# Optimization experiments

Measured on AMD Instinct MI355X. Metric: run time of the kernel, lower is better.

The kernel has to match this reference:

```python
import jax, jax.numpy as jnp
import numpy as np

B, T, D, U, OUT = 64, 1024, 512, 512, 4

def setup_inputs() -> dict:
    key = jax.random.key(0)
    ks = jax.random.split(key, 6)
    s = lambda n: 1.0 / np.sqrt(n)
    return {
        "tx": jax.random.normal(ks[0], (B, T, D), dtype=jnp.float32),
        "kernel": jax.random.normal(ks[1], (D, 4 * U), dtype=jnp.float32) * s(D),
        "recurrent_kernel": jax.random.normal(ks[2], (U, 4 * U), dtype=jnp.float32) * s(U),
        "bias": jnp.zeros((4 * U,), dtype=jnp.float32),
        "fc_w": jax.random.normal(ks[3], (U, OUT), dtype=jnp.float32) * s(U),
        "fc_b": jnp.zeros((OUT,), dtype=jnp.float32),
    }

def reference(tx, kernel, recurrent_kernel, bias, fc_w, fc_b):
    b, t, d = tx.shape
    u = recurrent_kernel.shape[0]
    # Fuse the 4 per-gate input matmuls into one GEMM over all timesteps: [B,T,4U]
    xz = jnp.einsum('btd,dk->btk', tx, kernel) + bias

    def step(carry, xz_t):
        h, c = carry
        z = xz_t + h @ recurrent_kernel  # fused 4 recurrent matmuls
        z1, z2, z3, z4 = jnp.split(z, 4, axis=-1)
        v1 = jnp.tanh(z1)
        v2 = jax.nn.sigmoid(z2)
        v3 = jax.nn.sigmoid(z3)
        v4 = jax.nn.sigmoid(z4)
        c = v1 * v2 + v3 * c
        h = v4 * jnp.tanh(c)
        return (h, c), None

    h0 = jnp.zeros((b, u), dtype=tx.dtype)
    c0 = jnp.zeros((b, u), dtype=tx.dtype)
    (h_last, _), _ = jax.lax.scan(step, (h0, c0), jnp.swapaxes(xz, 0, 1))
    # RNN(return_sequences=False) -> last hidden state, then Dense + softmax
    return jax.nn.softmax(h_last @ fc_w + fc_b, axis=-1)
```

## Files before the change

### kernel.cpp

```cpp
#include <hip/hip_runtime.h>
#include <stdint.h>

typedef short sv8 __attribute__((ext_vector_type(8)));
typedef float fv4 __attribute__((ext_vector_type(4)));
typedef uint32_t u32x4 __attribute__((ext_vector_type(4)));
typedef uint32_t u32x2 __attribute__((ext_vector_type(2)));

__device__ __forceinline__ uint16_t f2bf(float f) {
    uint32_t u = __builtin_bit_cast(uint32_t, f);
    u += 0x7FFFu + ((u >> 16) & 1u);
    return (uint16_t)(u >> 16);
}
__device__ __forceinline__ float bf2f(uint16_t h) {
    uint32_t u = ((uint32_t)h) << 16;
    return __builtin_bit_cast(float, u);
}
__device__ __forceinline__ void split4(float4 f, ushort4& h, ushort4& l) {
    h.x = f2bf(f.x); l.x = f2bf(f.x - bf2f(h.x));
    h.y = f2bf(f.y); l.y = f2bf(f.y - bf2f(h.y));
    h.z = f2bf(f.z); l.z = f2bf(f.z - bf2f(h.z));
    h.w = f2bf(f.w); l.w = f2bf(f.w - bf2f(h.w));
}
__device__ __forceinline__ float fsig(float x)  { return 1.f / (1.f + __expf(-x)); }
__device__ __forceinline__ float ftanh(float x) { return 1.f - 2.f / (__expf(2.f * x) + 1.f); }

__device__ __forceinline__ u32x4 load16_cc(const void* p) {
    u32x4 r;
    asm volatile("global_load_dwordx4 %0, %1, off sc0 sc1" : "=v"(r) : "v"(p) : "memory");
    return r;
}
__device__ __forceinline__ uint32_t load4_cc(const void* p) {
    uint32_t r;
    asm volatile("global_load_dword %0, %1, off sc0 sc1" : "=v"(r) : "v"(p) : "memory");
    return r;
}
__device__ __forceinline__ void atom8_st(void* p, u32x2 v) {
    asm volatile("global_atomic_swap_x2 %0, %1, off" :: "v"(p), "v"(v) : "memory");
}
__device__ __forceinline__ void atom4_st(void* p, uint32_t v) {
    asm volatile("global_atomic_swap %0, %1, off" :: "v"(p), "v"(v) : "memory");
}

#define TT     1024
#define DD     512
#define NN     2048
#define TCH    128
#define NCHUNK 8
#define NREG   8
#define RSTRIDE 16

__global__ void prep_split_b(const float* __restrict__ kern,
                             uint16_t* __restrict__ bth, uint16_t* __restrict__ btl) {
    int tid = blockIdx.x * 256 + threadIdx.x;
    if (tid >= DD * NN) return;
    int k = tid >> 11;
    int n = tid & (NN - 1);
    float v = kern[tid];
    uint16_t h = f2bf(v);
    bth[n * DD + k] = h;
    btl[n * DD + k] = f2bf(v - bf2f(h));
}

__global__ void prep_rk(const float* __restrict__ rk,
                        uint16_t* __restrict__ rkh, uint16_t* __restrict__ rkl) {
    int tid = blockIdx.x * 256 + threadIdx.x;
    if (tid >= 128 * 16 * 64 * 8) return;
    int j = tid & 7, lane = (tid >> 3) & 63, kt = (tid >> 9) & 15, g = tid >> 13;
    int lq = lane >> 4, c = lane & 15;
    int k = kt * 32 + lq * 8 + j;
    int colg = (c >> 2) * 512 + g * 4 + (c & 3);
    float v = rk[(size_t)k * NN + colg];
    uint16_t h = f2bf(v);
    rkh[tid] = h;
    rkl[tid] = f2bf(v - bf2f(h));
}

__device__ __forceinline__ void gemm_tile(
    const float* __restrict__ tx, int t0,
    const uint16_t* __restrict__ Bth, const uint16_t* __restrict__ Btl,
    float* __restrict__ xz, uint16_t* sb, int t256, int btile, int n0, int act) {
    int lane = t256 & 63, w = t256 >> 6;
    int wm = (w >> 1) * 64, wn = (w & 1) * 64;
    int srow = t256 >> 1, scol = (t256 & 1) * 16;
    fv4 acc[4][4];
#pragma unroll
    for (int q = 0; q < 4; q++)
#pragma unroll
        for (int r = 0; r < 4; r++) acc[q][r] = (fv4){0.f, 0.f, 0.f, 0.f};

    const float* abase = tx + ((size_t)btile * TT + t0 + srow) * DD + scol;

    for (int k0 = 0; k0 < DD; k0 += 32) {
        float4 f0, f1, f2, f3;
        uint4 b0, b1, c0, c1;
        if (act) {
            const float4* A4 = (const float4*)(abase + k0);
            f0 = A4[0]; f1 = A4[1]; f2 = A4[2]; f3 = A4[3];
            const uint16_t* pb  = Bth + (size_t)(n0 + srow) * DD + k0 + scol;
            const uint16_t* pbl = Btl + (size_t)(n0 + srow) * DD + k0 + scol;
            b0 = *(const uint4*)pb;  b1 = *(const uint4*)(pb + 8);
            c0 = *(const uint4*)pbl; c1 = *(const uint4*)(pbl + 8);
        }
        __syncthreads();
        if (act) {
            union { ushort4 v4[4]; uint4 q[2]; } H, L;
            split4(f0, H.v4[0], L.v4[0]);
            split4(f1, H.v4[1], L.v4[1]);
            split4(f2, H.v4[2], L.v4[2]);
            split4(f3, H.v4[3], L.v4[3]);
            *(uint4*)&sb[srow * 32 + scol]            = H.q[0];
            *(uint4*)&sb[srow * 32 + scol + 8]        = H.q[1];
            *(uint4*)&sb[4096 + srow * 32 + scol]     = L.q[0];
            *(uint4*)&sb[4096 + srow * 32 + scol + 8] = L.q[1];
            *(uint4*)&sb[8192 + srow * 32 + scol]     = b0;
            *(uint4*)&sb[8192 + srow * 32 + scol + 8] = b1;
            *(uint4*)&sb[12288 + srow * 32 + scol]    = c0;
            *(uint4*)&sb[12288 + srow * 32 + scol + 8]= c1;
        }
        __syncthreads();
        sv8 ah[4], al[4], bh[4], bl[4];
#pragma unroll
        for (int q = 0; q < 4; q++) {
            int ra = (wm + q * 16 + (lane & 15)) * 32 + (lane >> 4) * 8;
            ah[q] = *(const sv8*)&sb[ra];
            al[q] = *(const sv8*)&sb[4096 + ra];
        }
#pragma unroll
        for (int r = 0; r < 4; r++) {
            int rb = (wn + r * 16 + (lane & 15)) * 32 + (lane >> 4) * 8;
            bh[r] = *(const sv8*)&sb[8192 + rb];
            bl[r] = *(const sv8*)&sb[12288 + rb];
        }
#pragma unroll
        for (int q = 0; q < 4; q++)
#pragma unroll
            for (int r = 0; r < 4; r++) {
                acc[q][r] = __builtin_amdgcn_mfma_f32_16x16x32_bf16(ah[q], bh[r], acc[q][r], 0, 0, 0);
                acc[q][r] = __builtin_amdgcn_mfma_f32_16x16x32_bf16(ah[q], bl[r], acc[q][r], 0, 0, 0);
                acc[q][r] = __builtin_amdgcn_mfma_f32_16x16x32_bf16(al[q], bh[r], acc[q][r], 0, 0, 0);
            }
    }
    if (act) {
#pragma unroll
        for (int q = 0; q < 4; q++)
#pragma unroll
            for (int r = 0; r < 4; r++) {
                int tl0 = wm + q * 16 + ((lane >> 4) * 4);
                int ncol = n0 + wn + r * 16 + (lane & 15);
                int gate = ncol >> 9, uu = ncol & 511;
                int cil = gate * 4 + (uu & 3);
                int g = uu >> 2;
#pragma unroll
                for (int e = 0; e < 4; e++) {
                    size_t idx = (((size_t)(g * 64 + btile) * TCH + (tl0 + e)) << 4) + cil;
                    xz[idx] = acc[q][r][e];
                }
            }
    }
}

__global__ __launch_bounds__(256, 2) void gemm_xz(
    const float* __restrict__ tx, int t0,
    const uint16_t* __restrict__ Bth, const uint16_t* __restrict__ Btl,
    float* __restrict__ xz) {
    __shared__ __align__(16) uint16_t sb[16384];
    gemm_tile(tx, t0, Bth, Btl, xz, sb, threadIdx.x,
              blockIdx.x >> 4, (blockIdx.x & 15) * 128, 1);
}

__device__ __forceinline__ void lstm_body(
    const uint16_t* __restrict__ rkh, const uint16_t* __restrict__ rkl,
    const float* __restrict__ bias, const float* __restrict__ xz,
    char* __restrict__ hbuf, uint32_t* __restrict__ rdy,
    float* __restrict__ cstate, float* __restrict__ hlast, int gbase,
    uint16_t* ls , int wg, int tid) {
    int lane = tid & 63, w = tid >> 6;
    int wb = w >> 1, ct = w & 1;
    int c = lane & 15, lq = lane >> 4;
    int u = wg * 8 + ct * 4 + (c & 3);
    int g = u >> 2;
    int colg = (c >> 2) * 512 + u;

    sv8 BH[16], BL[16];
    {
        const sv8* ph = (const sv8*)rkh + (size_t)g * 1024 + lane;
        const sv8* pl = (const sv8*)rkl + (size_t)g * 1024 + lane;
#pragma unroll
        for (int kt = 0; kt < 16; kt++) {
            BH[kt] = ph[kt * 64];
            BL[kt] = pl[kt * 64];
        }
    }
    float bv = bias[colg];
    int b0 = wb * 16 + lq * 4;
    float cst[4];
#pragma unroll
    for (int r = 0; r < 4; r++) cst[r] = cstate[(b0 + r) * 512 + u];
    const float* xzb = xz + ((size_t)(g * 64 + b0) * TCH) * 16 + c;
    int off_w_short = ((wb * 16 + (wg >> 2)) * 64 + lq * 4 + 16 * (wg & 3)) * 8 + ct * 4;
    int own = (lane == wg) ? 1 : 0;

    for (int tl = 0; tl < TCH; tl++) {
        int t = gbase + tl;
        const float* xzt = xzb + tl * 16;
        float xzv[4];
#pragma unroll
        for (int r = 0; r < 4; r++) xzv[r] = xzt[r * (TCH * 16)];

        {
            const uint32_t* rp = rdy + (size_t)((t & (NREG - 1)) * 64 + lane) * RSTRIDE;
            uint32_t want = (uint32_t)t;
            for (;;) {
                uint32_t v = load4_cc(rp);
                asm volatile("s_waitcnt vmcnt(0)" ::: "memory");
                if (__all(own | (int)(v >= want))) break;
            }
        }
        const char* src = hbuf + (size_t)(t & (NREG - 1)) * 65536 + tid * 16;
        u32x4 hv[8];
#pragma unroll
        for (int i = 0; i < 8; i++) hv[i] = load16_cc(src + i * 8192);
        asm volatile("s_waitcnt vmcnt(0)" ::: "memory");
        __builtin_amdgcn_sched_barrier(0);
#pragma unroll
        for (int i = 0; i < 8; i++) *(u32x4*)&ls[i * 4096 + tid * 8] = hv[i];
        __syncthreads();

        fv4 aH = (fv4){0.f, 0.f, 0.f, 0.f};
        fv4 aL = (fv4){0.f, 0.f, 0.f, 0.f};
#pragma unroll
        for (int half = 0; half < 2; half++) {
            sv8 af[8];
#pragma unroll
            for (int k8 = 0; k8 < 8; k8++)
                af[k8] = *(const sv8*)&ls[((wb * 16 + half * 8 + k8) * 64 + lane) * 8];
#pragma unroll
            for (int k8 = 0; k8 < 8; k8++) {
                aH = __builtin_amdgcn_mfma_f32_16x16x32_bf16(af[k8], BH[half * 8 + k8], aH, 0, 0, 0);
                aL = __builtin_amdgcn_mfma_f32_16x16x32_bf16(af[k8], BL[half * 8 + k8], aL, 0, 0, 0);
            }
        }

        char* wdst = hbuf + (size_t)((t + 1) & (NREG - 1)) * 65536;
#pragma unroll
        for (int r = 0; r < 4; r++) {
            float z  = aH[r] + aL[r] + bv + xzv[r];
            float z2 = __shfl_xor(z, 4);
            float z3 = __shfl_xor(z, 8);
            float z4 = __shfl_xor(z, 12);
            float v1 = ftanh(z);
            float v2 = fsig(z2);
            float v3 = fsig(z3);
            float v4 = fsig(z4);
            cst[r] = v1 * v2 + v3 * cst[r];
            float hn = v4 * ftanh(cst[r]);
            uint32_t hbts = (uint32_t)f2bf(hn);
            int bsl = lane & 48;
            uint32_t h0 = __shfl(hbts, bsl);
            uint32_t h1 = __shfl(hbts, bsl + 1);
            uint32_t h2 = __shfl(hbts, bsl + 2);
            uint32_t h3 = __shfl(hbts, bsl + 3);
            if (c == 0) {
                u32x2 pk = (u32x2){h0 | (h1 << 16), h2 | (h3 << 16)};
                atom8_st(wdst + (size_t)(off_w_short + r * 8) * 2, pk);
            }
            if (t == TT - 1 && c < 4) hlast[(b0 + r) * 512 + u] = hn;
        }
        asm volatile("s_waitcnt vmcnt(0)" ::: "memory");
        __syncthreads();
        if (tid == 0)
            atom4_st(rdy + (size_t)(((t + 1) & (NREG - 1)) * 64 + wg) * RSTRIDE,
                     (uint32_t)(t + 1));
    }
    if (c < 4) {
#pragma unroll
        for (int r = 0; r < 4; r++) cstate[(b0 + r) * 512 + u] = cst[r];
    }
    asm volatile("s_waitcnt vmcnt(0)" ::: "memory");
}

__global__ __launch_bounds__(512, 1) void lstm_rec(
    const uint16_t* __restrict__ rkh, const uint16_t* __restrict__ rkl,
    const float* __restrict__ bias, const float* __restrict__ xz,
    char* __restrict__ hbuf, uint32_t* __restrict__ rdy,
    float* __restrict__ cstate, float* __restrict__ hlast, int gbase) {
    __shared__ __align__(16) uint16_t ls[32768];
    lstm_body(rkh, rkl, bias, xz, hbuf, rdy, cstate, hlast, gbase,
              ls, blockIdx.x, threadIdx.x);
}

__global__ __launch_bounds__(512, 1) void fused_step(
    const uint16_t* __restrict__ rkh, const uint16_t* __restrict__ rkl,
    const float* __restrict__ bias, const float* __restrict__ xz_cur,
    char* __restrict__ hbuf, uint32_t* __restrict__ rdy,
    float* __restrict__ cstate, float* __restrict__ hlast, int gbase,
    const float* __restrict__ tx, int t0_next,
    const uint16_t* __restrict__ Bth, const uint16_t* __restrict__ Btl,
    float* __restrict__ xz_next) {
    __shared__ __align__(16) uint16_t shm[32768];
    int bid = blockIdx.x, tid = threadIdx.x;
    if (bid < 64) {
        lstm_body(rkh, rkl, bias, xz_cur, hbuf, rdy, cstate, hlast, gbase,
                  shm, bid, tid);
    } else {
        if (t0_next < 0) return;
        int t256 = tid & 255, subwg = tid >> 8;
        uint16_t* sb = shm + subwg * 16384;
        int slot = (bid - 64) * 2 + subwg;
#pragma unroll 1
        for (int it = 0; it < 3; ++it) {
            int tile = slot + it * 384;
            int act = tile < 1024;
            int btile = (tile < 1024 ? tile : 0) >> 4;
            int n0 = ((tile < 1024 ? tile : 0) & 15) * 128;
            gemm_tile(tx, t0_next, Bth, Btl, xz_next, sb, t256, btile, n0, act);
        }
    }
}

__global__ void final_out(const float* __restrict__ hlast, const float* __restrict__ fcw,
                          const float* __restrict__ fcb, float* __restrict__ out) {
    __shared__ float lg[256];
    int tid = threadIdx.x;
    int b = tid >> 2, o = tid & 3;
    float s = fcb[o];
    const float* hr = hlast + b * 512;
    for (int k = 0; k < 512; k++) s += hr[k] * fcw[k * 4 + o];
    lg[tid] = s;
    __syncthreads();
    float l0 = lg[b * 4 + 0], l1 = lg[b * 4 + 1], l2 = lg[b * 4 + 2], l3 = lg[b * 4 + 3];
    float m = fmaxf(fmaxf(l0, l1), fmaxf(l2, l3));
    float sum = expf(l0 - m) + expf(l1 - m) + expf(l2 - m) + expf(l3 - m);
    out[tid] = expf(s - m) / sum;
}

extern "C" void kernel_launch(void* const* d_in, const int* in_sizes, int n_in,
                              void* d_out, int out_size, void* d_ws, size_t ws_size,
                              hipStream_t stream) {
    const float* tx   = (const float*)d_in[0];
    const float* kern = (const float*)d_in[1];
    const float* rk   = (const float*)d_in[2];
    const float* bias = (const float*)d_in[3];
    const float* fcw  = (const float*)d_in[4];
    const float* fcb  = (const float*)d_in[5];
    float* out = (float*)d_out;

    char* ws = (char*)d_ws;
    size_t off = 0;
    auto alloc = [&](size_t bytes) -> void* {
        void* p = ws + off;
        off += (bytes + 255) & ~(size_t)255;
        return p;
    };
    float*    xz0    = (float*)alloc((size_t)128 * 64 * TCH * 16 * 4);
    uint16_t* Bth    = (uint16_t*)alloc((size_t)NN * DD * 2);
    uint16_t* Btl    = (uint16_t*)alloc((size_t)NN * DD * 2);
    uint16_t* rkh    = (uint16_t*)alloc((size_t)128 * 16 * 64 * 8 * 2);
    uint16_t* rkl    = (uint16_t*)alloc((size_t)128 * 16 * 64 * 8 * 2);
    char*     hbuf   = (char*)alloc((size_t)NREG * 65536);
    uint32_t* rdy    = (uint32_t*)alloc((size_t)NREG * 64 * RSTRIDE * 4);
    float*    cstate = (float*)alloc(64 * 512 * 4);
    float*    hlast  = (float*)alloc(64 * 512 * 4);
    size_t small_need = off;
    float*    xz1    = (float*)alloc((size_t)128 * 64 * TCH * 16 * 4);
    size_t big_need = off;
    int big = (ws_size >= big_need);
    if (ws_size < small_need) big = 0;

    hipMemsetAsync(hbuf, 0, 65536, stream);
    hipMemsetAsync(rdy, 0, (size_t)NREG * 64 * RSTRIDE * 4, stream);
    hipMemsetAsync(cstate, 0, 64 * 512 * 4, stream);

    prep_split_b<<<4096, 256, 0, stream>>>(kern, Bth, Btl);
    prep_rk<<<4096, 256, 0, stream>>>(rk, rkh, rkl);

    if (big) {
        gemm_xz<<<1024, 256, 0, stream>>>(tx, 0, Bth, Btl, xz0);
        for (int k = 0; k < NCHUNK; ++k) {
            const float* xzc = (k & 1) ? xz1 : xz0;
            float*       xzn = (k & 1) ? xz0 : xz1;
            fused_step<<<256, 512, 0, stream>>>(rkh, rkl, bias, xzc, hbuf, rdy,
                                                cstate, hlast, k * TCH,
                                                tx, (k < NCHUNK - 1) ? (k + 1) * TCH : -1,
                                                Bth, Btl, xzn);
        }
    } else {
        for (int k = 0; k < NCHUNK; ++k) {
            gemm_xz<<<1024, 256, 0, stream>>>(tx, k * TCH, Bth, Btl, xz0);
            lstm_rec<<<64, 512, 0, stream>>>(rkh, rkl, bias, xz0, hbuf, rdy,
                                             cstate, hlast, k * TCH);
        }
    }
    final_out<<<1, 256, 0, stream>>>(hlast, fcw, fcb, out);
}
```

Measured before the change: 5.086 ms.

## Use per-wave readiness flags and direct global h loads in LSTM recurrence

The recurrent step now lets each wave load only the h rows it needs straight from global memory into MFMA operands, instead of staging all of h through LDS behind block barriers. Readiness flags become per-wave: each wave polls only the two producer waves it depends on and publishes its own flag without a __syncthreads. The first half of the MFMA work also overlaps with the second half of the loads. This targets the per-timestep barrier and LDS round-trip latency on the serial critical path, at the cost of more global polling traffic and redundant h loads across waves. Launch bounds are also changed to allow 2 blocks per CU.

```diff
diff --git a/kernel.cpp b/kernel.cpp
--- a/kernel.cpp
+++ b/kernel.cpp
@@ -27,11 +27,6 @@
 __device__ __forceinline__ u32x4 load16_cc(const void* p) {
     u32x4 r;
     asm volatile("global_load_dwordx4 %0, %1, off sc0 sc1" : "=v"(r) : "v"(p) : "memory");
-    return r;
-}
-__device__ __forceinline__ uint32_t load4_cc(const void* p) {
-    uint32_t r;
-    asm volatile("global_load_dword %0, %1, off sc0 sc1" : "=v"(r) : "v"(p) : "memory");
     return r;
 }
 __device__ __forceinline__ void atom8_st(void* p, u32x2 v) {
@@ -47,7 +42,6 @@
 #define TCH    128
 #define NCHUNK 8
 #define NREG   8
-#define RSTRIDE 16
 
 __global__ void prep_split_b(const float* __restrict__ kern,
                              uint16_t* __restrict__ bth, uint16_t* __restrict__ btl) {
@@ -173,7 +167,7 @@
     const float* __restrict__ bias, const float* __restrict__ xz,
     char* __restrict__ hbuf, uint32_t* __restrict__ rdy,
     float* __restrict__ cstate, float* __restrict__ hlast, int gbase,
-    uint16_t* ls , int wg, int tid) {
+    int wg, int tid) {
     int lane = tid & 63, w = tid >> 6;
     int wb = w >> 1, ct = w & 1;
     int c = lane & 15, lq = lane >> 4;
@@ -198,7 +192,6 @@
     for (int r = 0; r < 4; r++) cst[r] = cstate[(b0 + r) * 512 + u];
     const float* xzb = xz + ((size_t)(g * 64 + b0) * TCH) * 16 + c;
     int off_w_short = ((wb * 16 + (wg >> 2)) * 64 + lq * 4 + 16 * (wg & 3)) * 8 + ct * 4;
-    int own = (lane == wg) ? 1 : 0;
 
     for (int tl = 0; tl < TCH; tl++) {
         int t = gbase + tl;
@@ -208,37 +201,40 @@
         for (int r = 0; r < 4; r++) xzv[r] = xzt[r * (TCH * 16)];
 
         {
-            const uint32_t* rp = rdy + (size_t)((t & (NREG - 1)) * 64 + lane) * RSTRIDE;
+            const uint32_t* rp = rdy + (size_t)(t & (NREG - 1)) * 1024 + lane * 16 + wb * 2;
             uint32_t want = (uint32_t)t;
             for (;;) {
-                uint32_t v = load4_cc(rp);
+                u32x2 v;
+                asm volatile("global_load_dwordx2 %0, %1, off sc0 sc1"
+                             : "=v"(v) : "v"(rp) : "memory");
                 asm volatile("s_waitcnt vmcnt(0)" ::: "memory");
-                if (__all(own | (int)(v >= want))) break;
+                if (__all((int)(v[0] >= want && v[1] >= want))) break;
             }
         }
-        const char* src = hbuf + (size_t)(t & (NREG - 1)) * 65536 + tid * 16;
-        u32x4 hv[8];
-#pragma unroll
-        for (int i = 0; i < 8; i++) hv[i] = load16_cc(src + i * 8192);
+        const char* src = hbuf + (size_t)(t & (NREG - 1)) * 65536
+                        + (size_t)(wb * 16 * 64 + lane) * 16;
+        u32x4 afa[8], afb[8];
+#pragma unroll
+        for (int i = 0; i < 8; i++) afa[i] = load16_cc(src + i * 1024);
+#pragma unroll
+        for (int i = 0; i < 8; i++) afb[i] = load16_cc(src + (8 + i) * 1024);
+        fv4 aH = (fv4){0.f, 0.f, 0.f, 0.f};
+        fv4 aL = (fv4){0.f, 0.f, 0.f, 0.f};
+        asm volatile("s_waitcnt vmcnt(8)" ::: "memory");
+        __builtin_amdgcn_sched_barrier(0);
+#pragma unroll
+        for (int i = 0; i < 8; i++) {
+            sv8 a = __builtin_bit_cast(sv8, afa[i]);
+            aH = __builtin_amdgcn_mfma_f32_16x16x32_bf16(a, BH[i], aH, 0, 0, 0);
+            aL = __builtin_amdgcn_mfma_f32_16x16x32_bf16(a, BL[i], aL, 0, 0, 0);
+        }
         asm volatile("s_waitcnt vmcnt(0)" ::: "memory");
         __builtin_amdgcn_sched_barrier(0);
 #pragma unroll
-        for (int i = 0; i < 8; i++) *(u32x4*)&ls[i * 4096 + tid * 8] = hv[i];
-        __syncthreads();
-
-        fv4 aH = (fv4){0.f, 0.f, 0.f, 0.f};
-        fv4 aL = (fv4){0.f, 0.f, 0.f, 0.f};
-#pragma unroll
-        for (int half = 0; half < 2; half++) {
-            sv8 af[8];
-#pragma unroll
-            for (int k8 = 0; k8 < 8; k8++)
-                af[k8] = *(const sv8*)&ls[((wb * 16 + half * 8 + k8) * 64 + lane) * 8];
-#pragma unroll
-            for (int k8 = 0; k8 < 8; k8++) {
-                aH = __builtin_amdgcn_mfma_f32_16x16x32_bf16(af[k8], BH[half * 8 + k8], aH, 0, 0, 0);
-                aL = __builtin_amdgcn_mfma_f32_16x16x32_bf16(af[k8], BL[half * 8 + k8], aL, 0, 0, 0);
-            }
+        for (int i = 0; i < 8; i++) {
+            sv8 a = __builtin_bit_cast(sv8, afb[i]);
+            aH = __builtin_amdgcn_mfma_f32_16x16x32_bf16(a, BH[8 + i], aH, 0, 0, 0);
+            aL = __builtin_amdgcn_mfma_f32_16x16x32_bf16(a, BL[8 + i], aL, 0, 0, 0);
         }
 
         char* wdst = hbuf + (size_t)((t + 1) & (NREG - 1)) * 65536;
@@ -267,9 +263,8 @@
             if (t == TT - 1 && c < 4) hlast[(b0 + r) * 512 + u] = hn;
         }
         asm volatile("s_waitcnt vmcnt(0)" ::: "memory");
-        __syncthreads();
-        if (tid == 0)
-            atom4_st(rdy + (size_t)(((t + 1) & (NREG - 1)) * 64 + wg) * RSTRIDE,
+        if (lane == 0)
+            atom4_st(rdy + (size_t)((t + 1) & (NREG - 1)) * 1024 + wg * 16 + w,
                      (uint32_t)(t + 1));
     }
     if (c < 4) {
@@ -279,17 +274,16 @@
     asm volatile("s_waitcnt vmcnt(0)" ::: "memory");
 }
 
-__global__ __launch_bounds__(512, 1) void lstm_rec(
+__global__ __launch_bounds__(512, 2) void lstm_rec(
     const uint16_t* __restrict__ rkh, const uint16_t* __restrict__ rkl,
     const float* __restrict__ bias, const float* __restrict__ xz,
     char* __restrict__ hbuf, uint32_t* __restrict__ rdy,
     float* __restrict__ cstate, float* __restrict__ hlast, int gbase) {
-    __shared__ __align__(16) uint16_t ls[32768];
     lstm_body(rkh, rkl, bias, xz, hbuf, rdy, cstate, hlast, gbase,
-              ls, blockIdx.x, threadIdx.x);
-}
-
-__global__ __launch_bounds__(512, 1) void fused_step(
+              blockIdx.x, threadIdx.x);
+}
+
+__global__ __launch_bounds__(512, 2) void fused_step(
     const uint16_t* __restrict__ rkh, const uint16_t* __restrict__ rkl,
     const float* __restrict__ bias, const float* __restrict__ xz_cur,
     char* __restrict__ hbuf, uint32_t* __restrict__ rdy,
@@ -301,7 +295,7 @@
     int bid = blockIdx.x, tid = threadIdx.x;
     if (bid < 64) {
         lstm_body(rkh, rkl, bias, xz_cur, hbuf, rdy, cstate, hlast, gbase,
-                  shm, bid, tid);
+                  bid, tid);
     } else {
         if (t0_next < 0) return;
         int t256 = tid & 255, subwg = tid >> 8;
@@ -358,7 +352,7 @@
     uint16_t* rkh    = (uint16_t*)alloc((size_t)128 * 16 * 64 * 8 * 2);
     uint16_t* rkl    = (uint16_t*)alloc((size_t)128 * 16 * 64 * 8 * 2);
     char*     hbuf   = (char*)alloc((size_t)NREG * 65536);
-    uint32_t* rdy    = (uint32_t*)alloc((size_t)NREG * 64 * RSTRIDE * 4);
+    uint32_t* rdy    = (uint32_t*)alloc((size_t)NREG * 64 * 16 * 4);
     float*    cstate = (float*)alloc(64 * 512 * 4);
     float*    hlast  = (float*)alloc(64 * 512 * 4);
     size_t small_need = off;
@@ -368,7 +362,7 @@
     if (ws_size < small_need) big = 0;
 
     hipMemsetAsync(hbuf, 0, 65536, stream);
-    hipMemsetAsync(rdy, 0, (size_t)NREG * 64 * RSTRIDE * 4, stream);
+    hipMemsetAsync(rdy, 0, (size_t)NREG * 64 * 16 * 4, stream);
     hipMemsetAsync(cstate, 0, 64 * 512 * 4, stream);
 
     prep_split_b<<<4096, 256, 0, stream>>>(kern, Bth, Btl);
```

Result: slower. 7.085 ms (+39.3%).

## Shrink LSTM recurrence to 16 workgroups with each wave covering full batch

Applied to the files above, without the earlier changes.

The recurrent step now runs on 16 workgroups instead of 64. Each wave owns one gate group across all 64 batch rows, with four row tiles held in registers, so each wave issues four times more MFMAs per step but fewer workgroups take part in the per-step handshake. The ready-flag array shrinks to one packed 16-entry row per buffer slot, polled with a single 16-byte load per lane, and lstm waves get raised scheduling priority. More blocks are freed for the overlapped next-chunk GEMM, and launch bounds allow two blocks per CU. In exchange, the serial per-step critical path carries more compute per wave and more register pressure.

```diff
diff --git a/kernel.cpp b/kernel.cpp
--- a/kernel.cpp
+++ b/kernel.cpp
@@ -27,11 +27,6 @@
 __device__ __forceinline__ u32x4 load16_cc(const void* p) {
     u32x4 r;
     asm volatile("global_load_dwordx4 %0, %1, off sc0 sc1" : "=v"(r) : "v"(p) : "memory");
-    return r;
-}
-__device__ __forceinline__ uint32_t load4_cc(const void* p) {
-    uint32_t r;
-    asm volatile("global_load_dword %0, %1, off sc0 sc1" : "=v"(r) : "v"(p) : "memory");
     return r;
 }
 __device__ __forceinline__ void atom8_st(void* p, u32x2 v) {
@@ -47,7 +42,7 @@
 #define TCH    128
 #define NCHUNK 8
 #define NREG   8
-#define RSTRIDE 16
+#define NWG    16
 
 __global__ void prep_split_b(const float* __restrict__ kern,
                              uint16_t* __restrict__ bth, uint16_t* __restrict__ btl) {
@@ -174,12 +169,13 @@
     char* __restrict__ hbuf, uint32_t* __restrict__ rdy,
     float* __restrict__ cstate, float* __restrict__ hlast, int gbase,
     uint16_t* ls , int wg, int tid) {
+    __builtin_amdgcn_s_setprio(1);
     int lane = tid & 63, w = tid >> 6;
-    int wb = w >> 1, ct = w & 1;
     int c = lane & 15, lq = lane >> 4;
-    int u = wg * 8 + ct * 4 + (c & 3);
-    int g = u >> 2;
+    int g = wg * 8 + w;
+    int u = g * 4 + (c & 3);
     int colg = (c >> 2) * 512 + u;
+    int sel = (lane & 3) * 4;
 
     sv8 BH[16], BL[16];
     {
@@ -192,31 +188,43 @@
         }
     }
     float bv = bias[colg];
-    int b0 = wb * 16 + lq * 4;
-    float cst[4];
-#pragma unroll
-    for (int r = 0; r < 4; r++) cst[r] = cstate[(b0 + r) * 512 + u];
-    const float* xzb = xz + ((size_t)(g * 64 + b0) * TCH) * 16 + c;
-    int off_w_short = ((wb * 16 + (wg >> 2)) * 64 + lq * 4 + 16 * (wg & 3)) * 8 + ct * 4;
-    int own = (lane == wg) ? 1 : 0;
+    float cst[4][4];
+#pragma unroll
+    for (int rt = 0; rt < 4; rt++)
+#pragma unroll
+        for (int r = 0; r < 4; r++)
+            cst[rt][r] = cstate[(rt * 16 + lq * 4 + r) * 512 + u];
+    const float* xzbase = xz + ((size_t)g * 64 * TCH) * 16 + c;
+    int off_w = (wg * 64 + lq * 4 + 16 * ((w >> 1) & 3)) * 8 + (w & 1) * 4;
 
     for (int tl = 0; tl < TCH; tl++) {
         int t = gbase + tl;
-        const float* xzt = xzb + tl * 16;
-        float xzv[4];
-#pragma unroll
-        for (int r = 0; r < 4; r++) xzv[r] = xzt[r * (TCH * 16)];
+        int reg = t & (NREG - 1), wreg = (t + 1) & (NREG - 1);
+        float xzv[4][4];
+#pragma unroll
+        for (int rt = 0; rt < 4; rt++)
+#pragma unroll
+            for (int r = 0; r < 4; r++)
+                xzv[rt][r] = xzbase[((size_t)(rt * 16 + lq * 4 + r) * TCH + tl) * 16];
 
         {
-            const uint32_t* rp = rdy + (size_t)((t & (NREG - 1)) * 64 + lane) * RSTRIDE;
+            const uint32_t* rp = rdy + (reg << 4) + sel;
             uint32_t want = (uint32_t)t;
             for (;;) {
-                uint32_t v = load4_cc(rp);
+                u32x4 v;
+                asm volatile("global_load_dwordx4 %0, %1, off sc0 sc1"
+                             : "=v"(v) : "v"(rp) : "memory");
                 asm volatile("s_waitcnt vmcnt(0)" ::: "memory");
-                if (__all(own | (int)(v >= want))) break;
+                int ok = 1;
+#pragma unroll
+                for (int q = 0; q < 4; q++) {
+                    uint32_t wq = (sel + q == wg) ? 0u : want;
+                    ok &= (int)(v[q] >= wq);
+                }
+                if (__all(ok)) break;
             }
         }
-        const char* src = hbuf + (size_t)(t & (NREG - 1)) * 65536 + tid * 16;
+        const char* src = hbuf + (size_t)reg * 65536 + tid * 16;
         u32x4 hv[8];
 #pragma unroll
         for (int i = 0; i < 8; i++) hv[i] = load16_cc(src + i * 8192);
@@ -226,60 +234,65 @@
         for (int i = 0; i < 8; i++) *(u32x4*)&ls[i * 4096 + tid * 8] = hv[i];
         __syncthreads();
 
-        fv4 aH = (fv4){0.f, 0.f, 0.f, 0.f};
-        fv4 aL = (fv4){0.f, 0.f, 0.f, 0.f};
-#pragma unroll
-        for (int half = 0; half < 2; half++) {
-            sv8 af[8];
-#pragma unroll
-            for (int k8 = 0; k8 < 8; k8++)
-                af[k8] = *(const sv8*)&ls[((wb * 16 + half * 8 + k8) * 64 + lane) * 8];
-#pragma unroll
-            for (int k8 = 0; k8 < 8; k8++) {
-                aH = __builtin_amdgcn_mfma_f32_16x16x32_bf16(af[k8], BH[half * 8 + k8], aH, 0, 0, 0);
-                aL = __builtin_amdgcn_mfma_f32_16x16x32_bf16(af[k8], BL[half * 8 + k8], aL, 0, 0, 0);
+        fv4 aH[4], aL[4];
+#pragma unroll
+        for (int rt = 0; rt < 4; rt++) {
+            aH[rt] = (fv4){0.f, 0.f, 0.f, 0.f};
+            aL[rt] = (fv4){0.f, 0.f, 0.f, 0.f};
+        }
+#pragma unroll
+        for (int rt = 0; rt < 4; rt++)
+#pragma unroll
+            for (int kt = 0; kt < 16; kt++) {
+                sv8 af = *(const sv8*)&ls[((rt * 16 + kt) * 64 + lane) * 8];
+                aH[rt] = __builtin_amdgcn_mfma_f32_16x16x32_bf16(af, BH[kt], aH[rt], 0, 0, 0);
+                aL[rt] = __builtin_amdgcn_mfma_f32_16x16x32_bf16(af, BL[kt], aL[rt], 0, 0, 0);
             }
-        }
-
-        char* wdst = hbuf + (size_t)((t + 1) & (NREG - 1)) * 65536;
-#pragma unroll
-        for (int r = 0; r < 4; r++) {
-            float z  = aH[r] + aL[r] + bv + xzv[r];
-            float z2 = __shfl_xor(z, 4);
-            float z3 = __shfl_xor(z, 8);
-            float z4 = __shfl_xor(z, 12);
-            float v1 = ftanh(z);
-            float v2 = fsig(z2);
-            float v3 = fsig(z3);
-            float v4 = fsig(z4);
-            cst[r] = v1 * v2 + v3 * cst[r];
-            float hn = v4 * ftanh(cst[r]);
-            uint32_t hbts = (uint32_t)f2bf(hn);
-            int bsl = lane & 48;
-            uint32_t h0 = __shfl(hbts, bsl);
-            uint32_t h1 = __shfl(hbts, bsl + 1);
-            uint32_t h2 = __shfl(hbts, bsl + 2);
-            uint32_t h3 = __shfl(hbts, bsl + 3);
-            if (c == 0) {
-                u32x2 pk = (u32x2){h0 | (h1 << 16), h2 | (h3 << 16)};
-                atom8_st(wdst + (size_t)(off_w_short + r * 8) * 2, pk);
+
+        char* wdst = hbuf + (size_t)wreg * 65536;
+#pragma unroll
+        for (int rt = 0; rt < 4; rt++)
+#pragma unroll
+            for (int r = 0; r < 4; r++) {
+                float z  = aH[rt][r] + aL[rt][r] + bv + xzv[rt][r];
+                float z2 = __shfl_xor(z, 4);
+                float z3 = __shfl_xor(z, 8);
+                float z4 = __shfl_xor(z, 12);
+                float v1 = ftanh(z);
+                float v2 = fsig(z2);
+                float v3 = fsig(z3);
+                float v4 = fsig(z4);
+                cst[rt][r] = v1 * v2 + v3 * cst[rt][r];
+                float hn = v4 * ftanh(cst[rt][r]);
+                uint32_t hbts = (uint32_t)f2bf(hn);
+                int bsl = lane & 48;
+                uint32_t h0 = __shfl(hbts, bsl);
+                uint32_t h1 = __shfl(hbts, bsl + 1);
+                uint32_t h2 = __shfl(hbts, bsl + 2);
+                uint32_t h3 = __shfl(hbts, bsl + 3);
+                if (c == 0) {
+                    u32x2 pk = (u32x2){h0 | (h1 << 16), h2 | (h3 << 16)};
+                    atom8_st(wdst + (size_t)(off_w + rt * 8192 + r * 8) * 2, pk);
+                }
+                if (t == TT - 1 && c < 4)
+                    hlast[(rt * 16 + lq * 4 + r) * 512 + u] = hn;
             }
-            if (t == TT - 1 && c < 4) hlast[(b0 + r) * 512 + u] = hn;
-        }
         asm volatile("s_waitcnt vmcnt(0)" ::: "memory");
         __syncthreads();
         if (tid == 0)
-            atom4_st(rdy + (size_t)(((t + 1) & (NREG - 1)) * 64 + wg) * RSTRIDE,
-                     (uint32_t)(t + 1));
+            atom4_st(rdy + (wreg << 4) + wg, (uint32_t)(t + 1));
     }
     if (c < 4) {
 #pragma unroll
-        for (int r = 0; r < 4; r++) cstate[(b0 + r) * 512 + u] = cst[r];
+        for (int rt = 0; rt < 4; rt++)
+#pragma unroll
+            for (int r = 0; r < 4; r++)
+                cstate[(rt * 16 + lq * 4 + r) * 512 + u] = cst[rt][r];
     }
     asm volatile("s_waitcnt vmcnt(0)" ::: "memory");
 }
 
-__global__ __launch_bounds__(512, 1) void lstm_rec(
+__global__ __launch_bounds__(512, 2) void lstm_rec(
     const uint16_t* __restrict__ rkh, const uint16_t* __restrict__ rkl,
     const float* __restrict__ bias, const float* __restrict__ xz,
     char* __restrict__ hbuf, uint32_t* __restrict__ rdy,
@@ -289,7 +302,7 @@
               ls, blockIdx.x, threadIdx.x);
 }
 
-__global__ __launch_bounds__(512, 1) void fused_step(
+__global__ __launch_bounds__(512, 2) void fused_step(
     const uint16_t* __restrict__ rkh, const uint16_t* __restrict__ rkl,
     const float* __restrict__ bias, const float* __restrict__ xz_cur,
     char* __restrict__ hbuf, uint32_t* __restrict__ rdy,
@@ -299,17 +312,17 @@
     float* __restrict__ xz_next) {
     __shared__ __align__(16) uint16_t shm[32768];
     int bid = blockIdx.x, tid = threadIdx.x;
-    if (bid < 64) {
+    if (bid < NWG) {
         lstm_body(rkh, rkl, bias, xz_cur, hbuf, rdy, cstate, hlast, gbase,
                   shm, bid, tid);
     } else {
         if (t0_next < 0) return;
         int t256 = tid & 255, subwg = tid >> 8;
         uint16_t* sb = shm + subwg * 16384;
-        int slot = (bid - 64) * 2 + subwg;
+        int slot = (bid - NWG) * 2 + subwg;
 #pragma unroll 1
         for (int it = 0; it < 3; ++it) {
-            int tile = slot + it * 384;
+            int tile = slot + it * 480;
             int act = tile < 1024;
             int btile = (tile < 1024 ? tile : 0) >> 4;
             int n0 = ((tile < 1024 ? tile : 0) & 15) * 128;
@@ -358,7 +371,7 @@
     uint16_t* rkh    = (uint16_t*)alloc((size_t)128 * 16 * 64 * 8 * 2);
     uint16_t* rkl    = (uint16_t*)alloc((size_t)128 * 16 * 64 * 8 * 2);
     char*     hbuf   = (char*)alloc((size_t)NREG * 65536);
-    uint32_t* rdy    = (uint32_t*)alloc((size_t)NREG * 64 * RSTRIDE * 4);
+    uint32_t* rdy    = (uint32_t*)alloc((size_t)NREG * 16 * 4);
     float*    cstate = (float*)alloc(64 * 512 * 4);
     float*    hlast  = (float*)alloc(64 * 512 * 4);
     size_t small_need = off;
@@ -368,7 +381,7 @@
     if (ws_size < small_need) big = 0;
 
     hipMemsetAsync(hbuf, 0, 65536, stream);
-    hipMemsetAsync(rdy, 0, (size_t)NREG * 64 * RSTRIDE * 4, stream);
+    hipMemsetAsync(rdy, 0, (size_t)NREG * 16 * 4, stream);
     hipMemsetAsync(cstate, 0, 64 * 512 * 4, stream);
 
     prep_split_b<<<4096, 256, 0, stream>>>(kern, Bth, Btl);
@@ -387,7 +400,7 @@
     } else {
         for (int k = 0; k < NCHUNK; ++k) {
             gemm_xz<<<1024, 256, 0, stream>>>(tx, k * TCH, Bth, Btl, xz0);
-            lstm_rec<<<64, 512, 0, stream>>>(rkh, rkl, bias, xz0, hbuf, rdy,
+            lstm_rec<<<16, 512, 0, stream>>>(rkh, rkl, bias, xz0, hbuf, rdy,
                                              cstate, hlast, k * TCH);
         }
     }
```

Result: slower. 12.98 ms (+155.2%).

## Split LSTM recurrence into two independent batch halves with separate sync domains

Applied to the files above, without the earlier changes.

Partitions the 64 recurrent workgroups into two groups of 32. Each group handles half the batch (32 rows) and owns its own h ring buffer and ready-flag array. Each workgroup now covers 4 column groups for 32 batch rows, so it waits on only 32 peers and loads half as much h state per step. Launch bounds and LDS size change to allow 2 blocks per CU. This reduces cross-workgroup synchronization fan-in and per-step global traffic, at the cost of a different tile mapping and the risk of occupancy or register pressure changes.

```diff
diff --git a/kernel.cpp b/kernel.cpp
--- a/kernel.cpp
+++ b/kernel.cpp
@@ -48,6 +48,7 @@
 #define NCHUNK 8
 #define NREG   8
 #define RSTRIDE 16
+#define REGB   32768
 
 __global__ void prep_split_b(const float* __restrict__ kern,
                              uint16_t* __restrict__ bth, uint16_t* __restrict__ btl) {
@@ -174,11 +175,12 @@
     char* __restrict__ hbuf, uint32_t* __restrict__ rdy,
     float* __restrict__ cstate, float* __restrict__ hlast, int gbase,
     uint16_t* ls , int wg, int tid) {
+    int hf = wg >> 5, cg = wg & 31;
     int lane = tid & 63, w = tid >> 6;
-    int wb = w >> 1, ct = w & 1;
+    int wb = w >> 2, gq = w & 3;
     int c = lane & 15, lq = lane >> 4;
-    int u = wg * 8 + ct * 4 + (c & 3);
-    int g = u >> 2;
+    int g = cg * 4 + gq;
+    int u = g * 4 + (c & 3);
     int colg = (c >> 2) * 512 + u;
 
     sv8 BH[16], BL[16];
@@ -192,23 +194,27 @@
         }
     }
     float bv = bias[colg];
-    int b0 = wb * 16 + lq * 4;
+    int b0 = hf * 32 + wb * 16 + lq * 4;
     float cst[4];
 #pragma unroll
     for (int r = 0; r < 4; r++) cst[r] = cstate[(b0 + r) * 512 + u];
     const float* xzb = xz + ((size_t)(g * 64 + b0) * TCH) * 16 + c;
-    int off_w_short = ((wb * 16 + (wg >> 2)) * 64 + lq * 4 + 16 * (wg & 3)) * 8 + ct * 4;
-    int own = (lane == wg) ? 1 : 0;
+    int off_w = ((wb * 16 + (cg >> 1)) * 64 + lq * 4 + 16 * ((cg * 2 + (gq >> 1)) & 3)) * 8
+                + (gq & 1) * 4;
+    char*     hbx = hbuf + (size_t)hf * (NREG * REGB);
+    uint32_t* rdx = rdy + hf * (NREG * 32 * RSTRIDE);
+    int own = ((lane & 31) == cg) ? 1 : 0;
 
     for (int tl = 0; tl < TCH; tl++) {
         int t = gbase + tl;
+        int reg = t & (NREG - 1), wreg = (t + 1) & (NREG - 1);
         const float* xzt = xzb + tl * 16;
         float xzv[4];
 #pragma unroll
         for (int r = 0; r < 4; r++) xzv[r] = xzt[r * (TCH * 16)];
 
         {
-            const uint32_t* rp = rdy + (size_t)((t & (NREG - 1)) * 64 + lane) * RSTRIDE;
+            const uint32_t* rp = rdx + (size_t)(reg * 32 + (lane & 31)) * RSTRIDE;
             uint32_t want = (uint32_t)t;
             for (;;) {
                 uint32_t v = load4_cc(rp);
@@ -216,14 +222,14 @@
                 if (__all(own | (int)(v >= want))) break;
             }
         }
-        const char* src = hbuf + (size_t)(t & (NREG - 1)) * 65536 + tid * 16;
-        u32x4 hv[8];
-#pragma unroll
-        for (int i = 0; i < 8; i++) hv[i] = load16_cc(src + i * 8192);
+        const char* src = hbx + (size_t)reg * REGB + tid * 16;
+        u32x4 hv[4];
+#pragma unroll
+        for (int i = 0; i < 4; i++) hv[i] = load16_cc(src + i * 8192);
         asm volatile("s_waitcnt vmcnt(0)" ::: "memory");
         __builtin_amdgcn_sched_barrier(0);
 #pragma unroll
-        for (int i = 0; i < 8; i++) *(u32x4*)&ls[i * 4096 + tid * 8] = hv[i];
+        for (int i = 0; i < 4; i++) *(u32x4*)&ls[i * 4096 + tid * 8] = hv[i];
         __syncthreads();
 
         fv4 aH = (fv4){0.f, 0.f, 0.f, 0.f};
@@ -241,7 +247,7 @@
             }
         }
 
-        char* wdst = hbuf + (size_t)((t + 1) & (NREG - 1)) * 65536;
+        char* wdst = hbx + (size_t)wreg * REGB;
 #pragma unroll
         for (int r = 0; r < 4; r++) {
             float z  = aH[r] + aL[r] + bv + xzv[r];
@@ -262,15 +268,14 @@
             uint32_t h3 = __shfl(hbts, bsl + 3);
             if (c == 0) {
                 u32x2 pk = (u32x2){h0 | (h1 << 16), h2 | (h3 << 16)};
-                atom8_st(wdst + (size_t)(off_w_short + r * 8) * 2, pk);
+                atom8_st(wdst + (size_t)(off_w + r * 8) * 2, pk);
             }
             if (t == TT - 1 && c < 4) hlast[(b0 + r) * 512 + u] = hn;
         }
         asm volatile("s_waitcnt vmcnt(0)" ::: "memory");
         __syncthreads();
         if (tid == 0)
-            atom4_st(rdy + (size_t)(((t + 1) & (NREG - 1)) * 64 + wg) * RSTRIDE,
-                     (uint32_t)(t + 1));
+            atom4_st(rdx + (size_t)(wreg * 32 + cg) * RSTRIDE, (uint32_t)(t + 1));
     }
     if (c < 4) {
 #pragma unroll
@@ -279,17 +284,17 @@
     asm volatile("s_waitcnt vmcnt(0)" ::: "memory");
 }
 
-__global__ __launch_bounds__(512, 1) void lstm_rec(
+__global__ __launch_bounds__(512, 2) void lstm_rec(
     const uint16_t* __restrict__ rkh, const uint16_t* __restrict__ rkl,
     const float* __restrict__ bias, const float* __restrict__ xz,
     char* __restrict__ hbuf, uint32_t* __restrict__ rdy,
     float* __restrict__ cstate, float* __restrict__ hlast, int gbase) {
-    __shared__ __align__(16) uint16_t ls[32768];
+    __shared__ __align__(16) uint16_t ls[16384];
     lstm_body(rkh, rkl, bias, xz, hbuf, rdy, cstate, hlast, gbase,
               ls, blockIdx.x, threadIdx.x);
 }
 
-__global__ __launch_bounds__(512, 1) void fused_step(
+__global__ __launch_bounds__(512, 2) void fused_step(
     const uint16_t* __restrict__ rkh, const uint16_t* __restrict__ rkl,
     const float* __restrict__ bias, const float* __restrict__ xz_cur,
     char* __restrict__ hbuf, uint32_t* __restrict__ rdy,
@@ -357,8 +362,8 @@
     uint16_t* Btl    = (uint16_t*)alloc((size_t)NN * DD * 2);
     uint16_t* rkh    = (uint16_t*)alloc((size_t)128 * 16 * 64 * 8 * 2);
     uint16_t* rkl    = (uint16_t*)alloc((size_t)128 * 16 * 64 * 8 * 2);
-    char*     hbuf   = (char*)alloc((size_t)NREG * 65536);
-    uint32_t* rdy    = (uint32_t*)alloc((size_t)NREG * 64 * RSTRIDE * 4);
+    char*     hbuf   = (char*)alloc((size_t)2 * NREG * REGB);
+    uint32_t* rdy    = (uint32_t*)alloc((size_t)2 * NREG * 32 * RSTRIDE * 4);
     float*    cstate = (float*)alloc(64 * 512 * 4);
     float*    hlast  = (float*)alloc(64 * 512 * 4);
     size_t small_need = off;
@@ -367,8 +372,9 @@
     int big = (ws_size >= big_need);
     if (ws_size < small_need) big = 0;
 
-    hipMemsetAsync(hbuf, 0, 65536, stream);
-    hipMemsetAsync(rdy, 0, (size_t)NREG * 64 * RSTRIDE * 4, stream);
+    hipMemsetAsync(hbuf, 0, REGB, stream);
+    hipMemsetAsync(hbuf + (size_t)NREG * REGB, 0, REGB, stream);
+    hipMemsetAsync(rdy, 0, (size_t)2 * NREG * 32 * RSTRIDE * 4, stream);
     hipMemsetAsync(cstate, 0, 64 * 512 * 4, stream);
 
     prep_split_b<<<4096, 256, 0, stream>>>(kern, Bth, Btl);
```

Measured after the change: 4.604 ms. -9.5%, faster.
